# Performance work log

Hardware: AMD Instinct MI355X
Metric: run time of the kernel (lower is better)

Reference implementation:

```python
import jax, jax.numpy as jnp
import numpy as np
import math

IN_CH = 256
OUT_CH = 256
N_JOINTS = 25
BATCH = 16384


def setup_inputs() -> dict:
    key = jax.random.key(0)
    kx, kw = jax.random.split(key)
    x = jax.random.normal(kx, (N_JOINTS, BATCH, IN_CH), dtype=jnp.float32)
    stdv = 1.0 / math.sqrt(OUT_CH)
    weight = jax.random.uniform(kw, (IN_CH, OUT_CH), dtype=jnp.float32,
                                minval=-stdv, maxval=stdv)
    return {"x": x, "weight": weight}


def reference(x, weight):
    # x: (N, B, D) -> attention over joints N per batch element
    xb = jnp.transpose(x, (1, 0, 2))            # (B, N, D)
    s3 = jnp.einsum('bnd,bmd->bnm', xb, xb)     # (B, N, N) self-similarity
    s = jax.nn.softmax(s3, axis=-1)
    out = jnp.einsum('bnm,bmd->bnd', s, xb)     # (B, N, D)
    out = out @ weight                           # (B, N, out_channels)
    return out
```

## Files before the change

kernel.cpp:

```cpp
#include <hip/hip_runtime.h>

#define GRID   1024
#define BLOCK  256
#define BATCH  16384
#define NJ     25
#define DEPTH  256
#define ITERS  (BATCH / GRID)

typedef short s16x8 __attribute__((ext_vector_type(8)));
typedef short s16x4 __attribute__((ext_vector_type(4)));
typedef float f32x4 __attribute__((ext_vector_type(4)));

__device__ __forceinline__ short f2bf(float f) {
  union { float f; unsigned u; } c; c.f = f;
  unsigned r = (c.u + 0x7FFFu + ((c.u >> 16) & 1u)) >> 16;
  return (short)r;
}

#define MFMA(a, b, c) __builtin_amdgcn_mfma_f32_16x16x32_bf16((a), (b), (c), 0, 0, 0)

__global__ __launch_bounds__(BLOCK, 2)
void geo_gcn_fused(const float* __restrict__ x,
                   const float* __restrict__ w,
                   float* __restrict__ out)
{
  __shared__ short As[2][32][256];
  __shared__ float S3[2][32][36];
  __shared__ short Yt[4][64][32];

  const int tid  = threadIdx.x;
  const int wv   = tid >> 6;
  const int lane = tid & 63;
  const int quad = lane >> 4;
  const int l16  = lane & 15;

  s16x8 wf[8][4];
  {
    const int ncol = wv * 64 + l16;
#pragma unroll
    for (int ks = 0; ks < 8; ++ks)
#pragma unroll
      for (int td = 0; td < 4; ++td) {
        const float* wp = w + (size_t)(ks * 32 + quad * 8) * DEPTH + ncol + td * 16;
#pragma unroll
        for (int j = 0; j < 8; ++j)
          wf[ks][td][j] = f2bf(wp[(size_t)j * DEPTH]);
      }
  }

  const int tm_s = wv >> 1;
  const int tn_s = wv & 1;
  const int srow = tid >> 3;
  const int sq   = tid & 7;
  const int ssw  = (sq ^ (srow & 7)) * 8;

  const float* xb = x + (size_t)srow * BATCH * DEPTH + sq * 8;

  {
    const float* xp = xb + (size_t)blockIdx.x * DEPTH;
#pragma unroll
    for (int c = 0; c < 4; ++c) {
      float4 c0 = make_float4(0.f, 0.f, 0.f, 0.f), c1 = c0;
      if (srow < NJ) {
        c0 = *(const float4*)(xp + c * 64);
        c1 = *(const float4*)(xp + c * 64 + 4);
      }
      s16x8 h;
      h[0]=f2bf(c0.x); h[1]=f2bf(c0.y); h[2]=f2bf(c0.z); h[3]=f2bf(c0.w);
      h[4]=f2bf(c1.x); h[5]=f2bf(c1.y); h[6]=f2bf(c1.z); h[7]=f2bf(c1.w);
      *(s16x8*)&As[0][srow][ssw + c * 64] = h;
    }
  }
  __syncthreads();

  for (int ib = 0; ib < ITERS; ++ib) {
    const int b   = blockIdx.x + GRID * ib;
    const int buf = ib & 1;

    float4 nf[8];
#pragma unroll
    for (int i = 0; i < 8; ++i) nf[i] = make_float4(0.f, 0.f, 0.f, 0.f);
    if ((ib + 1 < ITERS) && (srow < NJ)) {
      const float* xp = xb + (size_t)(b + GRID) * DEPTH;
#pragma unroll
      for (int c = 0; c < 4; ++c) {
        nf[2 * c]     = *(const float4*)(xp + c * 64);
        nf[2 * c + 1] = *(const float4*)(xp + c * 64 + 4);
      }
    }

    f32x4 sacc = (f32x4){0.f, 0.f, 0.f, 0.f};
    f32x4 yacc[2][4];
#pragma unroll
    for (int i = 0; i < 2; ++i)
#pragma unroll
      for (int j = 0; j < 4; ++j) yacc[i][j] = (f32x4){0.f, 0.f, 0.f, 0.f};

#pragma unroll
    for (int ks = 0; ks < 8; ++ks) {
      const int co = (((ks * 4 + quad) ^ (l16 & 7)) << 3);
      s16x8 a0 = *(const s16x8*)&As[buf][l16][co];
      s16x8 a1 = *(const s16x8*)&As[buf][16 + l16][co];
      sacc = MFMA(tm_s ? a1 : a0, tn_s ? a1 : a0, sacc);
#pragma unroll
      for (int td = 0; td < 4; ++td) {
        yacc[0][td] = MFMA(a0, wf[ks][td], yacc[0][td]);
        yacc[1][td] = MFMA(a1, wf[ks][td], yacc[1][td]);
      }
    }

#pragma unroll
    for (int r = 0; r < 4; ++r)
      S3[buf][tm_s * 16 + quad * 4 + r][tn_s * 16 + l16] = sacc[r];

    if (ib + 1 < ITERS) {
#pragma unroll
      for (int c = 0; c < 4; ++c) {
        s16x8 h;
        h[0]=f2bf(nf[2*c].x);   h[1]=f2bf(nf[2*c].y);
        h[2]=f2bf(nf[2*c].z);   h[3]=f2bf(nf[2*c].w);
        h[4]=f2bf(nf[2*c+1].x); h[5]=f2bf(nf[2*c+1].y);
        h[6]=f2bf(nf[2*c+1].z); h[7]=f2bf(nf[2*c+1].w);
        *(s16x8*)&As[1 - buf][srow][ssw + c * 64] = h;
      }
    }
    __syncthreads();

    s16x8 pf0, pf1;
    {
      f32x4 v0a = *(const f32x4*)&S3[buf][l16][quad * 8];
      f32x4 v0b = *(const f32x4*)&S3[buf][l16][quad * 8 + 4];
      f32x4 v1a = *(const f32x4*)&S3[buf][16 + l16][quad * 8];
      f32x4 v1b = *(const f32x4*)&S3[buf][16 + l16][quad * 8 + 4];
      const float NINF = -3.0e38f;
      float mx0 = NINF, mx1 = NINF;
#pragma unroll
      for (int j = 0; j < 4; ++j) {
        const bool va = (quad * 8 + j) < NJ;
        const bool vb = (quad * 8 + 4 + j) < NJ;
        mx0 = fmaxf(mx0, va ? v0a[j] : NINF);
        mx0 = fmaxf(mx0, vb ? v0b[j] : NINF);
        mx1 = fmaxf(mx1, va ? v1a[j] : NINF);
        mx1 = fmaxf(mx1, vb ? v1b[j] : NINF);
      }
      mx0 = fmaxf(mx0, __shfl_xor(mx0, 16));
      mx0 = fmaxf(mx0, __shfl_xor(mx0, 32));
      mx1 = fmaxf(mx1, __shfl_xor(mx1, 16));
      mx1 = fmaxf(mx1, __shfl_xor(mx1, 32));
      float e0[8], e1[8], s0 = 0.f, s1 = 0.f;
#pragma unroll
      for (int j = 0; j < 4; ++j) {
        const bool va = (quad * 8 + j) < NJ;
        const bool vb = (quad * 8 + 4 + j) < NJ;
        e0[j]     = va ? __expf(v0a[j] - mx0) : 0.f;
        e0[j + 4] = vb ? __expf(v0b[j] - mx0) : 0.f;
        e1[j]     = va ? __expf(v1a[j] - mx1) : 0.f;
        e1[j + 4] = vb ? __expf(v1b[j] - mx1) : 0.f;
        s0 += e0[j] + e0[j + 4];
        s1 += e1[j] + e1[j + 4];
      }
      s0 += __shfl_xor(s0, 16);
      s0 += __shfl_xor(s0, 32);
      s1 += __shfl_xor(s1, 16);
      s1 += __shfl_xor(s1, 32);
      const float r0 = 1.0f / s0, r1 = 1.0f / s1;
#pragma unroll
      for (int j = 0; j < 8; ++j) {
        pf0[j] = f2bf(e0[j] * r0);
        pf1[j] = f2bf(e1[j] * r1);
      }
    }

#pragma unroll
    for (int tm = 0; tm < 2; ++tm)
#pragma unroll
      for (int td = 0; td < 4; ++td) {
        s16x4 hy;
#pragma unroll
        for (int r = 0; r < 4; ++r) hy[r] = f2bf(yacc[tm][td][r]);
        const int pc = (tm * 2 + (quad >> 1)) ^ ((l16 >> 1) & 3);
        *(s16x4*)&Yt[wv][td * 16 + l16][pc * 8 + (quad & 1) * 4] = hy;
      }

    const f32x4 z4 = (f32x4){0.f, 0.f, 0.f, 0.f};
    float* ob = out + (size_t)b * NJ * DEPTH + wv * 64 + l16;
#pragma unroll
    for (int td = 0; td < 4; ++td) {
      const int pr = quad ^ ((l16 >> 1) & 3);
      s16x8 yb = *(const s16x8*)&Yt[wv][td * 16 + l16][pr * 8];
      f32x4 o0 = MFMA(pf0, yb, z4);
      f32x4 o1 = MFMA(pf1, yb, z4);
#pragma unroll
      for (int r = 0; r < 4; ++r) {
        __builtin_nontemporal_store(o0[r], &ob[(size_t)(quad * 4 + r) * DEPTH + td * 16]);
        const int nr = 16 + quad * 4 + r;
        if (nr < NJ)
          __builtin_nontemporal_store(o1[r], &ob[(size_t)nr * DEPTH + td * 16]);
      }
    }
  }
}

extern "C" void kernel_launch(void* const* d_in, const int* in_sizes, int n_in,
                              void* d_out, int out_size, void* d_ws, size_t ws_size,
                              hipStream_t stream) {
  (void)in_sizes; (void)n_in; (void)out_size; (void)d_ws; (void)ws_size;
  const float* x = (const float*)d_in[0];
  const float* w = (const float*)d_in[1];
  float* out = (float*)d_out;
  geo_gcn_fused<<<dim3(GRID), dim3(BLOCK), 0, stream>>>(x, w, out);
}
```

Baseline: 753.2 us.

## Stream x into LDS via direct global-to-LDS loads and shuffle Y fragments

Prefetch of the next batch element now uses direct global-to-LDS DMA of fp32 rows with an XOR swizzle, replacing register staging and bf16 conversion before the LDS write. Conversion to bf16 moves to the MFMA operand read, and the LDS row size doubles. The Y tile transpose through LDS is replaced by cross-lane shuffles of packed bf16 pairs. Output stores drop the nontemporal hint. The aim is to free registers and VALU work from the load path and cut LDS traffic, at the cost of more LDS capacity and conversions repeated every step.

```diff
diff --git a/kernel.cpp b/kernel.cpp
--- a/kernel.cpp
+++ b/kernel.cpp
@@ -8,7 +8,6 @@
 #define ITERS  (BATCH / GRID)
 
 typedef short s16x8 __attribute__((ext_vector_type(8)));
-typedef short s16x4 __attribute__((ext_vector_type(4)));
 typedef float f32x4 __attribute__((ext_vector_type(4)));
 
 __device__ __forceinline__ short f2bf(float f) {
@@ -16,17 +15,26 @@
   unsigned r = (c.u + 0x7FFFu + ((c.u >> 16) & 1u)) >> 16;
   return (short)r;
 }
+__device__ __forceinline__ unsigned pk2(float lo, float hi) {
+  return ((unsigned)(unsigned short)f2bf(hi) << 16) |
+         (unsigned)(unsigned short)f2bf(lo);
+}
 
 #define MFMA(a, b, c) __builtin_amdgcn_mfma_f32_16x16x32_bf16((a), (b), (c), 0, 0, 0)
+
+__device__ __forceinline__ void dma16(const float* g, float* l) {
+  __builtin_amdgcn_global_load_lds(
+      (const __attribute__((address_space(1))) void*)g,
+      (__attribute__((address_space(3))) void*)l, 16, 0, 0);
+}
 
 __global__ __launch_bounds__(BLOCK, 2)
 void geo_gcn_fused(const float* __restrict__ x,
                    const float* __restrict__ w,
                    float* __restrict__ out)
 {
-  __shared__ short As[2][32][256];
+  __shared__ float Asf[2][32][256];
   __shared__ float S3[2][32][36];
-  __shared__ short Yt[4][64][32];
 
   const int tid  = threadIdx.x;
   const int wv   = tid >> 6;
@@ -50,25 +58,19 @@
 
   const int tm_s = wv >> 1;
   const int tn_s = wv & 1;
-  const int srow = tid >> 3;
-  const int sq   = tid & 7;
-  const int ssw  = (sq ^ (srow & 7)) * 8;
-
-  const float* xb = x + (size_t)srow * BATCH * DEPTH + sq * 8;
+  const int sA   = ((quad & 1) << 5) + l16;
+  const int sB   = sA + 16;
+  const bool lo32 = (lane < 32);
 
   {
-    const float* xp = xb + (size_t)blockIdx.x * DEPTH;
-#pragma unroll
-    for (int c = 0; c < 4; ++c) {
-      float4 c0 = make_float4(0.f, 0.f, 0.f, 0.f), c1 = c0;
-      if (srow < NJ) {
-        c0 = *(const float4*)(xp + c * 64);
-        c1 = *(const float4*)(xp + c * 64 + 4);
-      }
-      s16x8 h;
-      h[0]=f2bf(c0.x); h[1]=f2bf(c0.y); h[2]=f2bf(c0.z); h[3]=f2bf(c0.w);
-      h[4]=f2bf(c1.x); h[5]=f2bf(c1.y); h[6]=f2bf(c1.z); h[7]=f2bf(c1.w);
-      *(s16x8*)&As[0][srow][ssw + c * 64] = h;
+    const float* xe = x + (size_t)blockIdx.x * DEPTH;
+#pragma unroll
+    for (int j = 0; j < 8; ++j) {
+      const int r    = wv * 8 + j;
+      const int nrow = (r < NJ) ? r : (NJ - 1);
+      const float* src = xe + (size_t)nrow * BATCH * DEPTH
+                            + ((lane ^ (2 * (r & 7))) << 2);
+      dma16(src, &Asf[0][r][0]);
     }
   }
   __syncthreads();
@@ -77,15 +79,15 @@
     const int b   = blockIdx.x + GRID * ib;
     const int buf = ib & 1;
 
-    float4 nf[8];
-#pragma unroll
-    for (int i = 0; i < 8; ++i) nf[i] = make_float4(0.f, 0.f, 0.f, 0.f);
-    if ((ib + 1 < ITERS) && (srow < NJ)) {
-      const float* xp = xb + (size_t)(b + GRID) * DEPTH;
-#pragma unroll
-      for (int c = 0; c < 4; ++c) {
-        nf[2 * c]     = *(const float4*)(xp + c * 64);
-        nf[2 * c + 1] = *(const float4*)(xp + c * 64 + 4);
+    if (ib + 1 < ITERS) {
+      const float* xe = x + (size_t)(b + GRID) * DEPTH;
+#pragma unroll
+      for (int j = 0; j < 8; ++j) {
+        const int r    = wv * 8 + j;
+        const int nrow = (r < NJ) ? r : (NJ - 1);
+        const float* src = xe + (size_t)nrow * BATCH * DEPTH
+                              + ((lane ^ (2 * (r & 7))) << 2);
+        dma16(src, &Asf[1 - buf][r][0]);
       }
     }
 
@@ -98,9 +100,17 @@
 
 #pragma unroll
     for (int ks = 0; ks < 8; ++ks) {
-      const int co = (((ks * 4 + quad) ^ (l16 & 7)) << 3);
-      s16x8 a0 = *(const s16x8*)&As[buf][l16][co];
-      s16x8 a1 = *(const s16x8*)&As[buf][16 + l16][co];
+      const int g0 = (((4 * ks + quad) ^ (l16 & 7)) << 3);
+      f32x4 ra = *(const f32x4*)&Asf[buf][l16][g0];
+      f32x4 rb = *(const f32x4*)&Asf[buf][l16][g0 + 4];
+      f32x4 rc = *(const f32x4*)&Asf[buf][16 + l16][g0];
+      f32x4 rd = *(const f32x4*)&Asf[buf][16 + l16][g0 + 4];
+      s16x8 a0, a1;
+#pragma unroll
+      for (int j = 0; j < 4; ++j) {
+        a0[j] = f2bf(ra[j]); a0[4 + j] = f2bf(rb[j]);
+        a1[j] = f2bf(rc[j]); a1[4 + j] = f2bf(rd[j]);
+      }
       sacc = MFMA(tm_s ? a1 : a0, tn_s ? a1 : a0, sacc);
 #pragma unroll
       for (int td = 0; td < 4; ++td) {
@@ -113,17 +123,6 @@
     for (int r = 0; r < 4; ++r)
       S3[buf][tm_s * 16 + quad * 4 + r][tn_s * 16 + l16] = sacc[r];
 
-    if (ib + 1 < ITERS) {
-#pragma unroll
-      for (int c = 0; c < 4; ++c) {
-        s16x8 h;
-        h[0]=f2bf(nf[2*c].x);   h[1]=f2bf(nf[2*c].y);
-        h[2]=f2bf(nf[2*c].z);   h[3]=f2bf(nf[2*c].w);
-        h[4]=f2bf(nf[2*c+1].x); h[5]=f2bf(nf[2*c+1].y);
-        h[6]=f2bf(nf[2*c+1].z); h[7]=f2bf(nf[2*c+1].w);
-        *(s16x8*)&As[1 - buf][srow][ssw + c * 64] = h;
-      }
-    }
     __syncthreads();
 
     s16x8 pf0, pf1;
@@ -171,31 +170,29 @@
       }
     }
 
-#pragma unroll
-    for (int tm = 0; tm < 2; ++tm)
-#pragma unroll
-      for (int td = 0; td < 4; ++td) {
-        s16x4 hy;
-#pragma unroll
-        for (int r = 0; r < 4; ++r) hy[r] = f2bf(yacc[tm][td][r]);
-        const int pc = (tm * 2 + (quad >> 1)) ^ ((l16 >> 1) & 3);
-        *(s16x4*)&Yt[wv][td * 16 + l16][pc * 8 + (quad & 1) * 4] = hy;
-      }
-
     const f32x4 z4 = (f32x4){0.f, 0.f, 0.f, 0.f};
     float* ob = out + (size_t)b * NJ * DEPTH + wv * 64 + l16;
 #pragma unroll
     for (int td = 0; td < 4; ++td) {
-      const int pr = quad ^ ((l16 >> 1) & 3);
-      s16x8 yb = *(const s16x8*)&Yt[wv][td * 16 + l16][pr * 8];
-      f32x4 o0 = MFMA(pf0, yb, z4);
-      f32x4 o1 = MFMA(pf1, yb, z4);
+      const unsigned a0 = pk2(yacc[0][td][0], yacc[0][td][1]);
+      const unsigned a1 = pk2(yacc[0][td][2], yacc[0][td][3]);
+      const unsigned b0 = pk2(yacc[1][td][0], yacc[1][td][1]);
+      const unsigned b1 = pk2(yacc[1][td][2], yacc[1][td][3]);
+      union { unsigned u[4]; s16x8 v; } yu;
+      {
+        int u0, u1;
+        u0 = __shfl((int)a0, sA); u1 = __shfl((int)b0, sA); yu.u[0] = lo32 ? u0 : u1;
+        u0 = __shfl((int)a1, sA); u1 = __shfl((int)b1, sA); yu.u[1] = lo32 ? u0 : u1;
+        u0 = __shfl((int)a0, sB); u1 = __shfl((int)b0, sB); yu.u[2] = lo32 ? u0 : u1;
+        u0 = __shfl((int)a1, sB); u1 = __shfl((int)b1, sB); yu.u[3] = lo32 ? u0 : u1;
+      }
+      f32x4 o0 = MFMA(pf0, yu.v, z4);
+      f32x4 o1 = MFMA(pf1, yu.v, z4);
 #pragma unroll
       for (int r = 0; r < 4; ++r) {
-        __builtin_nontemporal_store(o0[r], &ob[(size_t)(quad * 4 + r) * DEPTH + td * 16]);
+        ob[(size_t)(quad * 4 + r) * DEPTH + td * 16] = o0[r];
         const int nr = 16 + quad * 4 + r;
-        if (nr < NJ)
-          __builtin_nontemporal_store(o1[r], &ob[(size_t)nr * DEPTH + td * 16]);
+        if (nr < NJ) ob[(size_t)nr * DEPTH + td * 16] = o1[r];
       }
     }
   }
```

Result: faster. 724.1 us (-3.9%).
